# Optimization experiments

Hardware: AMD Instinct MI355X
Metric: run time of the kernel (lower is better)

Reference implementation:

```python
import jax, jax.numpy as jnp
import numpy as np

NUM_CLASSES = 81
TOP_K = 200
CONF_THRESH = 0.01
NMS_THRESH = 0.45
VAR0, VAR1 = 0.1, 0.2  # SSD Config['variance']


def decode(loc, priors):
    # loc: [..., P, 4], priors: [P, 4] (cx, cy, w, h)
    cxcy = priors[:, :2] + loc[..., :2] * VAR0 * priors[:, 2:]
    wh = priors[:, 2:] * jnp.exp(loc[..., 2:] * VAR1)
    x1y1 = cxcy - wh * 0.5
    x2y2 = x1y1 + wh
    return jnp.concatenate([x1y1, x2y2], axis=-1)  # [..., P, 4] xyxy


def nms_class(boxes, scores):
    # boxes: [P, 4], scores: [P] -> [TOP_K, 5] rows of (score, x1, y1, x2, y2)
    K = TOP_K
    masked = jnp.where(scores > CONF_THRESH, scores, -jnp.inf)
    top_scores, idx = jax.lax.top_k(masked, K)          # descending
    cand = boxes[idx]                                   # [K, 4]
    valid = jnp.isfinite(top_scores)
    x1, y1, x2, y2 = cand[:, 0], cand[:, 1], cand[:, 2], cand[:, 3]
    area = (x2 - x1) * (y2 - y1)
    iw = jnp.maximum(jnp.minimum(x2[:, None], x2[None, :]) - jnp.maximum(x1[:, None], x1[None, :]), 0.0)
    ih = jnp.maximum(jnp.minimum(y2[:, None], y2[None, :]) - jnp.maximum(y1[:, None], y1[None, :]), 0.0)
    inter = iw * ih
    union = area[:, None] + area[None, :] - inter
    iou = jnp.where(union > 0, inter / jnp.where(union > 0, union, 1.0), 0.0)  # [K, K]
    ar = jnp.arange(K)

    def step(suppressed, i):
        kept = valid[i] & ~suppressed[i]
        suppressed = suppressed | (kept & (iou[i] > NMS_THRESH) & (ar > i))
        return suppressed, kept

    _, keep = jax.lax.scan(step, jnp.zeros(K, dtype=bool), ar)  # [K] bool
    rows = jnp.concatenate([jnp.where(valid, top_scores, 0.0)[:, None], cand], axis=1)  # [K, 5]
    # compact kept rows to the front (score-descending order), zeros after
    tgt = jnp.where(keep, jnp.cumsum(keep) - 1, K)
    out = jnp.zeros((K + 1, 5), rows.dtype).at[tgt].set(rows)[:K]
    return out


def detect(loc_data, conf_data, prior_data):
    boxes = decode(loc_data, prior_data)                 # [B, P, 4]
    conf = jnp.transpose(conf_data, (0, 2, 1))           # [B, C, P]
    per_image = jax.vmap(nms_class, in_axes=(None, 0))   # over classes
    out = jax.vmap(per_image, in_axes=(0, 0))(boxes, conf)  # [B, C, K, 5]
    out = out.at[:, 0].set(0.0)  # background class skipped (cl starts at 1)
    return out


def setup_inputs() -> dict:
    key = jax.random.key(0)
    k1, k2, k3 = jax.random.split(key, 3)
    B, P, C = 32, 24564, NUM_CLASSES
    loc_data = jax.random.normal(k1, (B, P, 4), dtype=jnp.float32)
    conf_data = jax.random.uniform(k2, (B, P, C), dtype=jnp.float32)
    prior_data = jax.random.uniform(k3, (P, 4), dtype=jnp.float32)
    return {"loc_data": loc_data, "conf_data": conf_data, "prior_data": prior_data}


def reference(loc_data, conf_data, prior_data):
    return detect(loc_data, conf_data, prior_data)
```

## Files before the change

### kernel.cpp

```cpp
#include <hip/hip_runtime.h>
#include <hip/hip_bf16.h>
#include <math.h>

constexpr int B_ = 32;
constexpr int P_ = 24564;
constexpr int C_ = 81;
constexpr int K_ = 200;

constexpr int NCH = 64;
constexpr int CPR = 384;
constexpr int SCAP = 1024;
constexpr int CAP  = 512;
constexpr float T_SEL = 0.9869f;

__global__ __launch_bounds__(256) void k_filter(const float* __restrict__ conf,
                                                unsigned long long* __restrict__ cand,
                                                unsigned* __restrict__ cnt,
                                                unsigned* __restrict__ bflag) {
    __shared__ unsigned long long skey[SCAP];
    __shared__ unsigned short scls[SCAP];
    __shared__ unsigned scnt[C_], sbase[C_], scnt2[C_];
    __shared__ unsigned sn;
    const int bid = blockIdx.x;
    const int b = bid / NCH, ch = bid % NCH;
    const int tid = threadIdx.x;

    for (int i = tid; i < C_; i += 256) { scnt[i] = 0; scnt2[i] = 0; }
    if (tid == 0) sn = 0;
    __syncthreads();

    const int p0 = ch * CPR;
    const int rows = min(CPR, P_ - p0);
    const float* slab = conf + ((size_t)b * P_ + (size_t)p0) * C_;
    const int n4 = rows * C_ / 4;
    for (int g = tid; g < n4; g += 256) {
        float4 v = ((const float4*)slab)[g];
        int e = g * 4;
        int c = e % C_;
        int pl = e / C_;
        float s[4] = {v.x, v.y, v.z, v.w};
#pragma unroll
        for (int j = 0; j < 4; ++j) {
            int cj = c + j, pj = pl;
            if (cj >= C_) { cj -= C_; pj += 1; }
            float sv = s[j];
            if (sv > T_SEL && cj != 0) {
                unsigned pos = atomicAdd(&sn, 1u);
                if (pos < (unsigned)SCAP) {
                    unsigned pg = (unsigned)(p0 + pj);
                    skey[pos] = ((unsigned long long)__float_as_uint(sv) << 32) | (~pg);
                    scls[pos] = (unsigned short)cj;
                    atomicAdd(&scnt[cj], 1u);
                } else {
                    bflag[b] = 1u;
                }
            }
        }
    }
    __syncthreads();
    if (tid < C_) sbase[tid] = scnt[tid] ? atomicAdd(&cnt[b * C_ + tid], scnt[tid]) : 0u;
    __syncthreads();
    const int m = (int)min(sn, (unsigned)SCAP);
    for (int i = tid; i < m; i += 256) {
        int c = scls[i];
        unsigned pos = sbase[c] + atomicAdd(&scnt2[c], 1u);
        if (pos < (unsigned)CAP)
            cand[((size_t)(b * C_ + c)) * CAP + pos] = skey[i];
    }
}

__global__ __launch_bounds__(256) void k_nms(const unsigned long long* __restrict__ cand,
                                             const unsigned* __restrict__ cnt,
                                             const unsigned* __restrict__ bflag,
                                             const float* __restrict__ conf,
                                             const float* __restrict__ loc,
                                             const float* __restrict__ prior,
                                             float* __restrict__ out) {
#pragma clang fp contract(off)
    __shared__ __align__(16) unsigned long long masks[K_][4];
    __shared__ __align__(16) float outrow[1024];
    __shared__ __align__(16) unsigned long long top[256];
    __shared__ __align__(16) float4 bbox[K_];
    __shared__ float sc[K_], bar[K_];
    __shared__ unsigned char vflag[K_];
    __shared__ unsigned long long keepw[4];
    __shared__ unsigned kpre[4];
    __shared__ unsigned long long sh_prefix;
    __shared__ unsigned sh_rank, sh_cnt2, sh_cut, sh_fat;

    unsigned long long* buf = (unsigned long long*)outrow;
    unsigned* rs_hist = (unsigned*)&masks[0][0];
    unsigned* rs_sf   = (unsigned*)&masks[32][0];
    unsigned long long* srt = &masks[64][0];

    const int bid = blockIdx.x;
    const int b = bid / C_, c = bid % C_;
    const int tid = threadIdx.x;
    float* obase = out + ((size_t)(b * C_ + c)) * (K_ * 5);

    if (c == 0) {
        float4 z = make_float4(0.f, 0.f, 0.f, 0.f);
        for (int i = tid; i < K_ * 5 / 4; i += 256) ((float4*)obase)[i] = z;
        return;
    }

    const int task = b * C_ + c;
    const unsigned long long* crow = cand + (size_t)task * CAP;
    const unsigned cn = cnt[task];
    const bool fb = (bflag[b] != 0u) || (cn < (unsigned)K_) || (cn > (unsigned)CAP);

    int n;
    if (!fb) {
        n = (int)cn;
        for (int i = tid; i < CAP; i += 256)
            buf[i] = (i < n) ? crow[i] : 0ull;
        top[tid] = 0ull;
        rs_hist[tid] = 0u;
        __syncthreads();
    } else {
        for (int i = tid; i < CAP; i += 256) buf[i] = 0ull;
        top[tid] = 0ull;
        const float* col = conf + (size_t)b * P_ * C_ + c;
        unsigned lc = 0;
        for (int p = tid; p < P_; p += 256)
            if (col[(size_t)p * C_] > 0.01f) lc++;
        rs_sf[tid] = lc;
        __syncthreads();
        for (int off = 128; off > 0; off >>= 1) {
            if (tid < off) rs_sf[tid] += rs_sf[tid + off];
            __syncthreads();
        }
        const unsigned total = rs_sf[0];
        unsigned long long t200v = 1ull;
        if (total > (unsigned)K_) {
            if (tid == 0) { sh_prefix = 0ull; sh_rank = (unsigned)K_; }
            __syncthreads();
            for (int d = 7; d >= 0; --d) {
                rs_hist[tid] = 0;
                __syncthreads();
                const unsigned long long pref = sh_prefix;
                const unsigned rank = sh_rank;
                for (int p = tid; p < P_; p += 256) {
                    float sv = col[(size_t)p * C_];
                    if (sv > 0.01f) {
                        unsigned long long key =
                            ((unsigned long long)__float_as_uint(sv) << 32) | (~(unsigned)p);
                        bool match = (d == 7) || (((key ^ pref) >> ((d + 1) * 8)) == 0ull);
                        if (match) atomicAdd(&rs_hist[(unsigned)((key >> (d * 8)) & 255ull)], 1u);
                    }
                }
                __syncthreads();
                rs_sf[tid] = rs_hist[tid];
                __syncthreads();
                for (int off = 1; off < 256; off <<= 1) {
                    unsigned v2 = (tid + off < 256) ? rs_sf[tid + off] : 0u;
                    __syncthreads();
                    rs_sf[tid] += v2;
                    __syncthreads();
                }
                if (rs_sf[tid] >= rank && (tid == 255 || rs_sf[tid + 1] < rank)) {
                    sh_prefix = pref | ((unsigned long long)tid << (d * 8));
                    sh_rank = rank - ((tid == 255) ? 0u : rs_sf[tid + 1]);
                }
                __syncthreads();
            }
            t200v = sh_prefix;
        }
        if (tid == 0) sh_cnt2 = 0;
        __syncthreads();
        for (int p = tid; p < P_; p += 256) {
            float sv = col[(size_t)p * C_];
            if (sv > 0.01f) {
                unsigned long long key =
                    ((unsigned long long)__float_as_uint(sv) << 32) | (~(unsigned)p);
                if (key >= t200v) {
                    unsigned pos = atomicAdd(&sh_cnt2, 1u);
                    if (pos < (unsigned)CAP) buf[pos] = key;
                }
            }
        }
        __syncthreads();
        n = (int)min(sh_cnt2, (unsigned)CAP);
    }

    bool fat = false;
    if (n <= 256) {
        top[tid] = (tid < n) ? buf[tid] : 0ull;
        __syncthreads();
    } else {
        for (int i = tid; i < n; i += 256)
            atomicAdd(&rs_hist[(unsigned)((buf[i] >> 43) & 255ull)], 1u);
        __syncthreads();
        if (tid < 64) {
            const int l = tid;
            uint4 h = *(const uint4*)&rs_hist[l * 4];
            unsigned s3 = h.w;
            unsigned s2 = h.z + s3;
            unsigned s1 = h.y + s2;
            unsigned s0 = h.x + s1;
            unsigned acc = s0;
            for (int off = 1; off < 64; off <<= 1) {
                unsigned o = __shfl_down(acc, off, 64);
                if (l + off < 64) acc += o;
            }
            const unsigned suf_after = acc - s0;
            unsigned long long bal = __ballot(s0 + suf_after >= (unsigned)K_);
            int hl = 63 - __builtin_clzll(bal);
            if (l == hl) {
                int k; unsigned sufk;
                if      (s3 + suf_after >= (unsigned)K_) { k = 3; sufk = s3 + suf_after; }
                else if (s2 + suf_after >= (unsigned)K_) { k = 2; sufk = s2 + suf_after; }
                else if (s1 + suf_after >= (unsigned)K_) { k = 1; sufk = s1 + suf_after; }
                else                                     { k = 0; sufk = s0 + suf_after; }
                sh_cut = (unsigned)(l * 4 + k);
                sh_fat = (sufk > 256u) ? 1u : 0u;
                sh_cnt2 = 0u;
            }
        }
        __syncthreads();
        fat = (sh_fat != 0u);
        if (!fat) {
            const unsigned cut = sh_cut;
            for (int i = tid; i < n; i += 256) {
                unsigned long long key = buf[i];
                if ((unsigned)((key >> 43) & 255ull) >= cut)
                    top[atomicAdd(&sh_cnt2, 1u)] = key;
            }
            __syncthreads();
        }
    }

    if (!fat) {
        const unsigned long long k1 = top[tid];
        int r1 = 0;
        for (int i = 0; i < 256; i += 4) {
            ulonglong2 a  = *(const ulonglong2*)&top[i];
            ulonglong2 b2 = *(const ulonglong2*)&top[i + 2];
            r1 += (a.x > k1) + (a.y > k1) + (b2.x > k1) + (b2.y > k1);
        }
        if (k1 != 0ull) srt[r1] = k1;
    } else {
        const unsigned long long k1 = buf[tid];
        const unsigned long long k2 = buf[tid + 256];
        int r1 = 0, r2 = 0;
        for (int i = 0; i < 512; i += 4) {
            ulonglong2 a  = *(const ulonglong2*)&buf[i];
            ulonglong2 b2 = *(const ulonglong2*)&buf[i + 2];
            r1 += (a.x > k1) + (a.y > k1) + (b2.x > k1) + (b2.y > k1);
            r2 += (a.x > k2) + (a.y > k2) + (b2.x > k2) + (b2.y > k2);
        }
        if (k1 != 0ull && r1 < 256) srt[r1] = k1;
        if (k2 != 0ull && r2 < 256) srt[r2] = k2;
    }
    __syncthreads();

    const int nsel = min(n, K_);

    if (tid < K_) {
        const int r = tid;
        bool v = (r < nsel);
        float score = 0.f, x1 = 0.f, y1 = 0.f, x2 = 0.f, y2 = 0.f, ar = 0.f;
        if (v) {
            unsigned long long key = srt[r];
            unsigned ub = (unsigned)(key >> 32);
            unsigned p = ~((unsigned)key);
            score = __uint_as_float(ub);
            v = ((ub & 0x7F800000u) != 0x7F800000u);
            const float4 l4 = ((const float4*)loc)[(size_t)b * P_ + p];
            const float4 p4 = ((const float4*)prior)[p];
            float cx = p4.x + (l4.x * 0.1f) * p4.z;
            float cy = p4.y + (l4.y * 0.1f) * p4.w;
            float w  = p4.z * expf(l4.z * 0.2f);
            float h  = p4.w * expf(l4.w * 0.2f);
            x1 = cx - w * 0.5f;
            y1 = cy - h * 0.5f;
            x2 = x1 + w;
            y2 = y1 + h;
            ar = (x2 - x1) * (y2 - y1);
        }
        bbox[r] = make_float4(x1, y1, x2, y2);
        sc[r] = score; bar[r] = ar;
        vflag[r] = v ? (unsigned char)1 : (unsigned char)0;
    }
    __syncthreads();

    {
        float4 z = make_float4(0.f, 0.f, 0.f, 0.f);
        ((float4*)outrow)[tid] = z;
    }

    const int nv = nsel;
    const int wid = tid >> 6, lane = tid & 63;

    float4 jb[4]; float jar[4];
#pragma unroll
    for (int w = 0; w < 4; ++w) {
        int j = w * 64 + lane;
        bool in = (j < K_);
        jb[w]  = in ? bbox[j] : make_float4(0.f, 0.f, 0.f, 0.f);
        jar[w] = in ? bar[j] : 0.f;
    }

    for (int idx = tid; idx < K_ * 4; idx += 256) {
        int i = idx >> 2, w = idx & 3;
        if (w < (i >> 6)) masks[i][w] = 0ull;
    }
    for (int i = wid; i < nv; i += 4) {
        float4 rb = bbox[i];
        float r_ar = bar[i];
        const int w0 = i >> 6;
#pragma unroll
        for (int w = 0; w < 4; ++w) {
            if (w >= w0) {
                int j = w * 64 + lane;
                bool pred = false;
                if (j < nv && j > i) {
                    float xx1 = fmaxf(rb.x, jb[w].x);
                    float yy1 = fmaxf(rb.y, jb[w].y);
                    float xx2 = fminf(rb.z, jb[w].z);
                    float yy2 = fminf(rb.w, jb[w].w);
                    float iw = fmaxf(xx2 - xx1, 0.0f);
                    float ih = fmaxf(yy2 - yy1, 0.0f);
                    float inter = iw * ih;
                    float uni = (r_ar + jar[w]) - inter;
                    pred = (uni > 0.0f) && (inter / uni > 0.45f);
                }
                unsigned long long m = __ballot(pred);
                if (lane == 0) masks[i][w] = m;
            }
        }
    }
    __syncthreads();

    if (tid < 64) {
        const int l = tid;
        unsigned long long V0 = __ballot((l       < nv) && vflag[l]);
        unsigned long long V1 = __ballot((64 + l  < nv) && vflag[64 + l]);
        unsigned long long V2 = __ballot((128 + l < nv) && vflag[128 + l]);
        unsigned long long V3 = __ballot((192 + l < nv) && vflag[192 + l]);
        auto rownz = [&](int r) -> bool {
            if (r >= nv) return false;
            return (masks[r][0] | masks[r][1] | masks[r][2] | masks[r][3]) != 0ull;
        };
        unsigned long long R0 = __ballot(rownz(l))       & V0;
        unsigned long long R1 = __ballot(rownz(64 + l))  & V1;
        unsigned long long R2 = __ballot(rownz(128 + l)) & V2;
        unsigned long long R3 = __ballot(rownz(192 + l)) & V3;

        unsigned long long S0 = 0, S1 = 0, S2 = 0, S3 = 0;
        while (true) {
            unsigned long long t;
            int i = -1;
            if ((t = R0 & ~S0) != 0ull)      i = (int)__builtin_ctzll(t);
            else if ((t = R1 & ~S1) != 0ull) i = 64 + (int)__builtin_ctzll(t);
            else if ((t = R2 & ~S2) != 0ull) i = 128 + (int)__builtin_ctzll(t);
            else if ((t = R3 & ~S3) != 0ull) i = 192 + (int)__builtin_ctzll(t);
            if (i < 0) break;
            const unsigned long long bit = 1ull << (i & 63);
            const int slot = i >> 6;
            if (slot == 0) R0 ^= bit; else if (slot == 1) R1 ^= bit;
            else if (slot == 2) R2 ^= bit; else R3 ^= bit;
            ulonglong2 m01 = *(const ulonglong2*)&masks[i][0];
            ulonglong2 m23 = *(const ulonglong2*)&masks[i][2];
            S0 |= m01.x; S1 |= m01.y; S2 |= m23.x; S3 |= m23.y;
        }
        if (l == 0) {
            unsigned long long K0 = V0 & ~S0, K1 = V1 & ~S1, K2 = V2 & ~S2, K3 = V3 & ~S3;
            keepw[0] = K0; keepw[1] = K1; keepw[2] = K2; keepw[3] = K3;
            kpre[0] = 0;
            kpre[1] = (unsigned)__popcll(K0);
            kpre[2] = kpre[1] + (unsigned)__popcll(K1);
            kpre[3] = kpre[2] + (unsigned)__popcll(K2);
        }
    }
    __syncthreads();

    if (tid < nv) {
        int w = tid >> 6, bit = tid & 63;
        if ((keepw[w] >> bit) & 1ull) {
            unsigned slot = kpre[w] + (unsigned)__popcll(keepw[w] & ((1ull << bit) - 1ull));
            float4 bb = bbox[tid];
            outrow[slot * 5 + 0] = sc[tid];
            outrow[slot * 5 + 1] = bb.x;
            outrow[slot * 5 + 2] = bb.y;
            outrow[slot * 5 + 3] = bb.z;
            outrow[slot * 5 + 4] = bb.w;
        }
    }
    __syncthreads();

    for (int i = tid; i < K_ * 5 / 4; i += 256)
        ((float4*)obase)[i] = ((const float4*)outrow)[i];
}

extern "C" void kernel_launch(void* const* d_in, const int* in_sizes, int n_in,
                              void* d_out, int out_size, void* d_ws, size_t ws_size,
                              hipStream_t stream) {
    const float* loc   = (const float*)d_in[0];
    const float* conf  = (const float*)d_in[1];
    const float* prior = (const float*)d_in[2];
    float* out = (float*)d_out;

    char* ws = (char*)d_ws;
    const size_t candBytes = (size_t)B_ * C_ * CAP * sizeof(unsigned long long);
    unsigned long long* cand = (unsigned long long*)ws;
    unsigned* cnt   = (unsigned*)(ws + candBytes);
    unsigned* bflag = cnt + (size_t)B_ * C_;

    hipMemsetAsync(cnt, 0, (size_t)(B_ * C_ + B_) * sizeof(unsigned), stream);

    k_filter<<<B_ * NCH, 256, 0, stream>>>(conf, cand, cnt, bflag);
    k_nms   <<<B_ * C_,  256, 0, stream>>>(cand, cnt, bflag, conf, loc, prior, out);
}
```

Baseline: 156.7 us.

## Replace precomputed IoU mask matrix with on-the-fly greedy NMS in one wave

Drops the full K×K suppression-bitmask build and instead runs greedy NMS in a single wavefront, computing IoU only for rows that are actually kept and clearing suppressed bits via ballot. It also ranks candidates on the 32-bit score word with a tie-break pass, decodes boxes directly at their rank without an intermediate sorted array, compacts warp-wide with ballot instead of per-element atomics, and writes output straight to global memory while zero-filling only the tail. The cost removed is redundant IoU work and the extra shared-memory passes. In exchange the NMS loop becomes serial over kept boxes on just 64 threads, which could lengthen the critical path when many boxes are kept.

```diff
diff --git a/kernel.cpp b/kernel.cpp
--- a/kernel.cpp
+++ b/kernel.cpp
@@ -77,9 +77,9 @@
                                              const float* __restrict__ prior,
                                              float* __restrict__ out) {
 #pragma clang fp contract(off)
-    __shared__ __align__(16) unsigned long long masks[K_][4];
-    __shared__ __align__(16) float outrow[1024];
+    __shared__ __align__(16) unsigned long long buf[CAP];
     __shared__ __align__(16) unsigned long long top[256];
+    __shared__ __align__(16) unsigned shi[256];
     __shared__ __align__(16) float4 bbox[K_];
     __shared__ float sc[K_], bar[K_];
     __shared__ unsigned char vflag[K_];
@@ -88,14 +88,13 @@
     __shared__ unsigned long long sh_prefix;
     __shared__ unsigned sh_rank, sh_cnt2, sh_cut, sh_fat;
 
-    unsigned long long* buf = (unsigned long long*)outrow;
-    unsigned* rs_hist = (unsigned*)&masks[0][0];
-    unsigned* rs_sf   = (unsigned*)&masks[32][0];
-    unsigned long long* srt = &masks[64][0];
+    unsigned* rs_hist = (unsigned*)&bbox[0];
+    unsigned* rs_sf   = (unsigned*)&bbox[64];
 
     const int bid = blockIdx.x;
     const int b = bid / C_, c = bid % C_;
     const int tid = threadIdx.x;
+    const int lane = tid & 63;
     float* obase = out + ((size_t)(b * C_ + c)) * (K_ * 5);
 
     if (c == 0) {
@@ -110,16 +109,70 @@
     const bool fb = (bflag[b] != 0u) || (cn < (unsigned)K_) || (cn > (unsigned)CAP);
 
     int n;
+    bool fat = false;
     if (!fb) {
         n = (int)cn;
-        for (int i = tid; i < CAP; i += 256)
-            buf[i] = (i < n) ? crow[i] : 0ull;
-        top[tid] = 0ull;
-        rs_hist[tid] = 0u;
-        __syncthreads();
+        if (n <= 256) {
+            unsigned long long k = (tid < n) ? crow[tid] : 0ull;
+            top[tid] = k; shi[tid] = (unsigned)(k >> 32);
+            __syncthreads();
+        } else {
+            for (int i = tid; i < CAP; i += 256) buf[i] = (i < n) ? crow[i] : 0ull;
+            top[tid] = 0ull; shi[tid] = 0u; rs_hist[tid] = 0u;
+            __syncthreads();
+            for (int i = tid; i < n; i += 256)
+                atomicAdd(&rs_hist[(unsigned)((buf[i] >> 43) & 255ull)], 1u);
+            __syncthreads();
+            if (tid < 64) {
+                const int l = tid;
+                uint4 h = *(const uint4*)&rs_hist[l * 4];
+                unsigned s3 = h.w;
+                unsigned s2 = h.z + s3;
+                unsigned s1 = h.y + s2;
+                unsigned s0 = h.x + s1;
+                unsigned acc = s0;
+                for (int off = 1; off < 64; off <<= 1) {
+                    unsigned o = __shfl_down(acc, off, 64);
+                    if (l + off < 64) acc += o;
+                }
+                const unsigned suf_after = acc - s0;
+                unsigned long long bal = __ballot(s0 + suf_after >= (unsigned)K_);
+                int hl = 63 - __builtin_clzll(bal);
+                if (l == hl) {
+                    int k; unsigned sufk;
+                    if      (s3 + suf_after >= (unsigned)K_) { k = 3; sufk = s3 + suf_after; }
+                    else if (s2 + suf_after >= (unsigned)K_) { k = 2; sufk = s2 + suf_after; }
+                    else if (s1 + suf_after >= (unsigned)K_) { k = 1; sufk = s1 + suf_after; }
+                    else                                     { k = 0; sufk = s0 + suf_after; }
+                    sh_cut = (unsigned)(l * 4 + k);
+                    sh_fat = (sufk > 256u) ? 1u : 0u;
+                    sh_cnt2 = 0u;
+                }
+            }
+            __syncthreads();
+            fat = (sh_fat != 0u);
+            if (!fat) {
+                const unsigned cut = sh_cut;
+#pragma unroll
+                for (int base = 0; base < CAP; base += 256) {
+                    int i = base + tid;
+                    unsigned long long key = buf[i];
+                    bool q = (i < n) && ((unsigned)((key >> 43) & 255ull) >= cut);
+                    unsigned long long bal = __ballot(q);
+                    unsigned pre = (unsigned)__popcll(bal & ((1ull << lane) - 1ull));
+                    unsigned wb = 0;
+                    if (lane == 0) {
+                        unsigned cw = (unsigned)__popcll(bal);
+                        if (cw) wb = atomicAdd(&sh_cnt2, cw);
+                    }
+                    wb = (unsigned)__shfl((int)wb, 0, 64);
+                    if (q) { top[wb + pre] = key; shi[wb + pre] = (unsigned)(key >> 32); }
+                }
+                __syncthreads();
+            }
+        }
     } else {
         for (int i = tid; i < CAP; i += 256) buf[i] = 0ull;
-        top[tid] = 0ull;
         const float* col = conf + (size_t)b * P_ * C_ + c;
         unsigned lc = 0;
         for (int p = tid; p < P_; p += 256)
@@ -181,140 +234,113 @@
         }
         __syncthreads();
         n = (int)min(sh_cnt2, (unsigned)CAP);
-    }
-
-    bool fat = false;
-    if (n <= 256) {
-        top[tid] = (tid < n) ? buf[tid] : 0ull;
+        unsigned long long k = (tid < n) ? buf[tid] : 0ull;
+        top[tid] = k; shi[tid] = (unsigned)(k >> 32);
         __syncthreads();
-    } else {
-        for (int i = tid; i < n; i += 256)
-            atomicAdd(&rs_hist[(unsigned)((buf[i] >> 43) & 255ull)], 1u);
-        __syncthreads();
-        if (tid < 64) {
-            const int l = tid;
-            uint4 h = *(const uint4*)&rs_hist[l * 4];
-            unsigned s3 = h.w;
-            unsigned s2 = h.z + s3;
-            unsigned s1 = h.y + s2;
-            unsigned s0 = h.x + s1;
-            unsigned acc = s0;
-            for (int off = 1; off < 64; off <<= 1) {
-                unsigned o = __shfl_down(acc, off, 64);
-                if (l + off < 64) acc += o;
-            }
-            const unsigned suf_after = acc - s0;
-            unsigned long long bal = __ballot(s0 + suf_after >= (unsigned)K_);
-            int hl = 63 - __builtin_clzll(bal);
-            if (l == hl) {
-                int k; unsigned sufk;
-                if      (s3 + suf_after >= (unsigned)K_) { k = 3; sufk = s3 + suf_after; }
-                else if (s2 + suf_after >= (unsigned)K_) { k = 2; sufk = s2 + suf_after; }
-                else if (s1 + suf_after >= (unsigned)K_) { k = 1; sufk = s1 + suf_after; }
-                else                                     { k = 0; sufk = s0 + suf_after; }
-                sh_cut = (unsigned)(l * 4 + k);
-                sh_fat = (sufk > 256u) ? 1u : 0u;
-                sh_cnt2 = 0u;
-            }
-        }
-        __syncthreads();
-        fat = (sh_fat != 0u);
-        if (!fat) {
-            const unsigned cut = sh_cut;
-            for (int i = tid; i < n; i += 256) {
-                unsigned long long key = buf[i];
-                if ((unsigned)((key >> 43) & 255ull) >= cut)
-                    top[atomicAdd(&sh_cnt2, 1u)] = key;
-            }
-            __syncthreads();
-        }
-    }
+    }
+
+    const int nsel = min(n, K_);
+
+    auto decode_to = [&](unsigned long long key, int r) {
+        unsigned ub = (unsigned)(key >> 32);
+        unsigned p = ~((unsigned)key);
+        float score = __uint_as_float(ub);
+        bool v = ((ub & 0x7F800000u) != 0x7F800000u);
+        const float4 l4 = ((const float4*)loc)[(size_t)b * P_ + p];
+        const float4 p4 = ((const float4*)prior)[p];
+        float cx = p4.x + (l4.x * 0.1f) * p4.z;
+        float cy = p4.y + (l4.y * 0.1f) * p4.w;
+        float w  = p4.z * expf(l4.z * 0.2f);
+        float h  = p4.w * expf(l4.w * 0.2f);
+        float x1 = cx - w * 0.5f;
+        float y1 = cy - h * 0.5f;
+        float x2 = x1 + w;
+        float y2 = y1 + h;
+        bbox[r] = make_float4(x1, y1, x2, y2);
+        sc[r] = score;
+        bar[r] = (x2 - x1) * (y2 - y1);
+        vflag[r] = v ? (unsigned char)1 : (unsigned char)0;
+    };
 
     if (!fat) {
         const unsigned long long k1 = top[tid];
-        int r1 = 0;
-        for (int i = 0; i < 256; i += 4) {
-            ulonglong2 a  = *(const ulonglong2*)&top[i];
-            ulonglong2 b2 = *(const ulonglong2*)&top[i + 2];
-            r1 += (a.x > k1) + (a.y > k1) + (b2.x > k1) + (b2.y > k1);
-        }
-        if (k1 != 0ull) srt[r1] = k1;
+        const unsigned khi = (unsigned)(k1 >> 32);
+        int r1 = 0, eq = 0;
+        for (int i = 0; i < 256; i += 8) {
+            uint4 a = *(const uint4*)&shi[i];
+            uint4 d = *(const uint4*)&shi[i + 4];
+            r1 += (a.x > khi) + (a.y > khi) + (a.z > khi) + (a.w > khi)
+                + (d.x > khi) + (d.y > khi) + (d.z > khi) + (d.w > khi);
+            eq += (a.x == khi) + (a.y == khi) + (a.z == khi) + (a.w == khi)
+                + (d.x == khi) + (d.y == khi) + (d.z == khi) + (d.w == khi);
+        }
+        if (__any(k1 != 0ull && eq > 1)) {
+            const unsigned klo = (unsigned)k1;
+            for (int i = 0; i < 256; i += 4) {
+                ulonglong2 a = *(const ulonglong2*)&top[i];
+                ulonglong2 d = *(const ulonglong2*)&top[i + 2];
+                r1 += ((unsigned)(a.x >> 32) == khi) && ((unsigned)a.x > klo);
+                r1 += ((unsigned)(a.y >> 32) == khi) && ((unsigned)a.y > klo);
+                r1 += ((unsigned)(d.x >> 32) == khi) && ((unsigned)d.x > klo);
+                r1 += ((unsigned)(d.y >> 32) == khi) && ((unsigned)d.y > klo);
+            }
+        }
+        if (k1 != 0ull && r1 < K_) decode_to(k1, r1);
     } else {
         const unsigned long long k1 = buf[tid];
         const unsigned long long k2 = buf[tid + 256];
         int r1 = 0, r2 = 0;
-        for (int i = 0; i < 512; i += 4) {
-            ulonglong2 a  = *(const ulonglong2*)&buf[i];
-            ulonglong2 b2 = *(const ulonglong2*)&buf[i + 2];
-            r1 += (a.x > k1) + (a.y > k1) + (b2.x > k1) + (b2.y > k1);
-            r2 += (a.x > k2) + (a.y > k2) + (b2.x > k2) + (b2.y > k2);
-        }
-        if (k1 != 0ull && r1 < 256) srt[r1] = k1;
-        if (k2 != 0ull && r2 < 256) srt[r2] = k2;
+        for (int i = 0; i < CAP; i += 4) {
+            ulonglong2 a = *(const ulonglong2*)&buf[i];
+            ulonglong2 d = *(const ulonglong2*)&buf[i + 2];
+            r1 += (a.x > k1) + (a.y > k1) + (d.x > k1) + (d.y > k1);
+            r2 += (a.x > k2) + (a.y > k2) + (d.x > k2) + (d.y > k2);
+        }
+        if (k1 != 0ull && r1 < K_) decode_to(k1, r1);
+        if (k2 != 0ull && r2 < K_) decode_to(k2, r2);
+    }
+    if (tid >= nsel && tid < K_) {
+        bbox[tid] = make_float4(0.f, 0.f, 0.f, 0.f);
+        sc[tid] = 0.f; bar[tid] = 0.f; vflag[tid] = 0;
     }
     __syncthreads();
 
-    const int nsel = min(n, K_);
-
-    if (tid < K_) {
-        const int r = tid;
-        bool v = (r < nsel);
-        float score = 0.f, x1 = 0.f, y1 = 0.f, x2 = 0.f, y2 = 0.f, ar = 0.f;
-        if (v) {
-            unsigned long long key = srt[r];
-            unsigned ub = (unsigned)(key >> 32);
-            unsigned p = ~((unsigned)key);
-            score = __uint_as_float(ub);
-            v = ((ub & 0x7F800000u) != 0x7F800000u);
-            const float4 l4 = ((const float4*)loc)[(size_t)b * P_ + p];
-            const float4 p4 = ((const float4*)prior)[p];
-            float cx = p4.x + (l4.x * 0.1f) * p4.z;
-            float cy = p4.y + (l4.y * 0.1f) * p4.w;
-            float w  = p4.z * expf(l4.z * 0.2f);
-            float h  = p4.w * expf(l4.w * 0.2f);
-            x1 = cx - w * 0.5f;
-            y1 = cy - h * 0.5f;
-            x2 = x1 + w;
-            y2 = y1 + h;
-            ar = (x2 - x1) * (y2 - y1);
-        }
-        bbox[r] = make_float4(x1, y1, x2, y2);
-        sc[r] = score; bar[r] = ar;
-        vflag[r] = v ? (unsigned char)1 : (unsigned char)0;
-    }
-    __syncthreads();
-
-    {
-        float4 z = make_float4(0.f, 0.f, 0.f, 0.f);
-        ((float4*)outrow)[tid] = z;
-    }
-
-    const int nv = nsel;
-    const int wid = tid >> 6, lane = tid & 63;
-
-    float4 jb[4]; float jar[4];
-#pragma unroll
-    for (int w = 0; w < 4; ++w) {
-        int j = w * 64 + lane;
-        bool in = (j < K_);
-        jb[w]  = in ? bbox[j] : make_float4(0.f, 0.f, 0.f, 0.f);
-        jar[w] = in ? bar[j] : 0.f;
-    }
-
-    for (int idx = tid; idx < K_ * 4; idx += 256) {
-        int i = idx >> 2, w = idx & 3;
-        if (w < (i >> 6)) masks[i][w] = 0ull;
-    }
-    for (int i = wid; i < nv; i += 4) {
-        float4 rb = bbox[i];
-        float r_ar = bar[i];
-        const int w0 = i >> 6;
+    if (tid < 64) {
+        const int l = tid;
+        float4 jb[4]; float jar[4];
 #pragma unroll
         for (int w = 0; w < 4; ++w) {
-            if (w >= w0) {
-                int j = w * 64 + lane;
+            int j = w * 64 + l;
+            bool in = (j < K_);
+            jb[w]  = in ? bbox[j] : make_float4(0.f, 0.f, 0.f, 0.f);
+            jar[w] = in ? bar[j] : 0.f;
+        }
+        unsigned long long A0 = __ballot(vflag[l] != 0);
+        unsigned long long A1 = __ballot(vflag[64 + l] != 0);
+        unsigned long long A2 = __ballot(vflag[128 + l] != 0);
+        unsigned long long A3 = __ballot((192 + l < K_) && vflag[192 + l]);
+        unsigned long long K0 = 0, K1m = 0, K2m = 0, K3m = 0;
+
+        while (A0 | A1 | A2 | A3) {
+            int i;
+            if (A0)      i = (int)__builtin_ctzll(A0);
+            else if (A1) i = 64 + (int)__builtin_ctzll(A1);
+            else if (A2) i = 128 + (int)__builtin_ctzll(A2);
+            else         i = 192 + (int)__builtin_ctzll(A3);
+            const unsigned long long bit = 1ull << (i & 63);
+            const int slot = i >> 6;
+            if (slot == 0)      { A0 ^= bit; K0 |= bit; }
+            else if (slot == 1) { A1 ^= bit; K1m |= bit; }
+            else if (slot == 2) { A2 ^= bit; K2m |= bit; }
+            else                { A3 ^= bit; K3m |= bit; }
+
+            float4 rb = bbox[i];
+            float rar = bar[i];
+#pragma unroll
+            for (int w = 0; w < 4; ++w) {
+                int j = w * 64 + l;
                 bool pred = false;
-                if (j < nv && j > i) {
+                if (j > i) {
                     float xx1 = fmaxf(rb.x, jb[w].x);
                     float yy1 = fmaxf(rb.y, jb[w].y);
                     float xx2 = fminf(rb.z, jb[w].z);
@@ -322,75 +348,41 @@
                     float iw = fmaxf(xx2 - xx1, 0.0f);
                     float ih = fmaxf(yy2 - yy1, 0.0f);
                     float inter = iw * ih;
-                    float uni = (r_ar + jar[w]) - inter;
+                    float uni = (rar + jar[w]) - inter;
                     pred = (uni > 0.0f) && (inter / uni > 0.45f);
                 }
-                unsigned long long m = __ballot(pred);
-                if (lane == 0) masks[i][w] = m;
-            }
-        }
-    }
-    __syncthreads();
-
-    if (tid < 64) {
-        const int l = tid;
-        unsigned long long V0 = __ballot((l       < nv) && vflag[l]);
-        unsigned long long V1 = __ballot((64 + l  < nv) && vflag[64 + l]);
-        unsigned long long V2 = __ballot((128 + l < nv) && vflag[128 + l]);
-        unsigned long long V3 = __ballot((192 + l < nv) && vflag[192 + l]);
-        auto rownz = [&](int r) -> bool {
-            if (r >= nv) return false;
-            return (masks[r][0] | masks[r][1] | masks[r][2] | masks[r][3]) != 0ull;
-        };
-        unsigned long long R0 = __ballot(rownz(l))       & V0;
-        unsigned long long R1 = __ballot(rownz(64 + l))  & V1;
-        unsigned long long R2 = __ballot(rownz(128 + l)) & V2;
-        unsigned long long R3 = __ballot(rownz(192 + l)) & V3;
-
-        unsigned long long S0 = 0, S1 = 0, S2 = 0, S3 = 0;
-        while (true) {
-            unsigned long long t;
-            int i = -1;
-            if ((t = R0 & ~S0) != 0ull)      i = (int)__builtin_ctzll(t);
-            else if ((t = R1 & ~S1) != 0ull) i = 64 + (int)__builtin_ctzll(t);
-            else if ((t = R2 & ~S2) != 0ull) i = 128 + (int)__builtin_ctzll(t);
-            else if ((t = R3 & ~S3) != 0ull) i = 192 + (int)__builtin_ctzll(t);
-            if (i < 0) break;
-            const unsigned long long bit = 1ull << (i & 63);
-            const int slot = i >> 6;
-            if (slot == 0) R0 ^= bit; else if (slot == 1) R1 ^= bit;
-            else if (slot == 2) R2 ^= bit; else R3 ^= bit;
-            ulonglong2 m01 = *(const ulonglong2*)&masks[i][0];
-            ulonglong2 m23 = *(const ulonglong2*)&masks[i][2];
-            S0 |= m01.x; S1 |= m01.y; S2 |= m23.x; S3 |= m23.y;
+                unsigned long long bw = __ballot(pred);
+                if (w == 0) A0 &= ~bw;
+                else if (w == 1) A1 &= ~bw;
+                else if (w == 2) A2 &= ~bw;
+                else A3 &= ~bw;
+            }
         }
         if (l == 0) {
-            unsigned long long K0 = V0 & ~S0, K1 = V1 & ~S1, K2 = V2 & ~S2, K3 = V3 & ~S3;
-            keepw[0] = K0; keepw[1] = K1; keepw[2] = K2; keepw[3] = K3;
+            keepw[0] = K0; keepw[1] = K1m; keepw[2] = K2m; keepw[3] = K3m;
             kpre[0] = 0;
             kpre[1] = (unsigned)__popcll(K0);
-            kpre[2] = kpre[1] + (unsigned)__popcll(K1);
-            kpre[3] = kpre[2] + (unsigned)__popcll(K2);
+            kpre[2] = kpre[1] + (unsigned)__popcll(K1m);
+            kpre[3] = kpre[2] + (unsigned)__popcll(K2m);
         }
     }
     __syncthreads();
 
-    if (tid < nv) {
+    if (tid < K_) {
         int w = tid >> 6, bit = tid & 63;
         if ((keepw[w] >> bit) & 1ull) {
             unsigned slot = kpre[w] + (unsigned)__popcll(keepw[w] & ((1ull << bit) - 1ull));
             float4 bb = bbox[tid];
-            outrow[slot * 5 + 0] = sc[tid];
-            outrow[slot * 5 + 1] = bb.x;
-            outrow[slot * 5 + 2] = bb.y;
-            outrow[slot * 5 + 3] = bb.z;
-            outrow[slot * 5 + 4] = bb.w;
-        }
-    }
-    __syncthreads();
-
-    for (int i = tid; i < K_ * 5 / 4; i += 256)
-        ((float4*)obase)[i] = ((const float4*)outrow)[i];
+            float* o = obase + slot * 5;
+            o[0] = sc[tid]; o[1] = bb.x; o[2] = bb.y; o[3] = bb.z; o[4] = bb.w;
+        }
+    }
+    {
+        const unsigned keptTotal = kpre[3] + (unsigned)__popcll(keepw[3]);
+        const int zbase = (int)keptTotal * 5;
+        const int ztot = K_ * 5 - zbase;
+        for (int e = tid; e < ztot; e += 256) obase[zbase + e] = 0.0f;
+    }
 }
 
 extern "C" void kernel_launch(void* const* d_in, const int* in_sizes, int n_in,
```

Measured after the change: 212.5 us. 35.6% more time.

## Keep candidates in registers, fuse rank-sort with decode, write output directly

Applied to the files above, without the earlier changes.

In the fast path each thread now keeps its candidate keys in registers instead of staging them through shared memory. Compaction uses wave ballot plus one atomic per wave rather than per-element atomics. The rank computation writes decoded boxes straight into their sorted slot, which removes the separate srt array and one barrier. The shared outrow staging buffer is gone: kept rows go directly to global memory and only the tail is zero-filled. The IoU test switches from a float divide to a double-precision compare against a midpoint threshold, which trades the divide for double arithmetic while aiming to reproduce the float rounding.

```diff
diff --git a/kernel.cpp b/kernel.cpp
--- a/kernel.cpp
+++ b/kernel.cpp
@@ -78,7 +78,6 @@
                                              float* __restrict__ out) {
 #pragma clang fp contract(off)
     __shared__ __align__(16) unsigned long long masks[K_][4];
-    __shared__ __align__(16) float outrow[1024];
     __shared__ __align__(16) unsigned long long top[256];
     __shared__ __align__(16) float4 bbox[K_];
     __shared__ float sc[K_], bar[K_];
@@ -88,14 +87,14 @@
     __shared__ unsigned long long sh_prefix;
     __shared__ unsigned sh_rank, sh_cnt2, sh_cut, sh_fat;
 
-    unsigned long long* buf = (unsigned long long*)outrow;
-    unsigned* rs_hist = (unsigned*)&masks[0][0];
-    unsigned* rs_sf   = (unsigned*)&masks[32][0];
-    unsigned long long* srt = &masks[64][0];
+    unsigned long long* buf = &masks[0][0];
+    unsigned* rs_hist = (unsigned*)&masks[128][0];
+    unsigned* rs_sf   = (unsigned*)&masks[160][0];
 
     const int bid = blockIdx.x;
     const int b = bid / C_, c = bid % C_;
     const int tid = threadIdx.x;
+    const int lane = tid & 63;
     float* obase = out + ((size_t)(b * C_ + c)) * (K_ * 5);
 
     if (c == 0) {
@@ -110,16 +109,85 @@
     const bool fb = (bflag[b] != 0u) || (cn < (unsigned)K_) || (cn > (unsigned)CAP);
 
     int n;
+    bool fat = false;
     if (!fb) {
         n = (int)cn;
-        for (int i = tid; i < CAP; i += 256)
-            buf[i] = (i < n) ? crow[i] : 0ull;
-        top[tid] = 0ull;
-        rs_hist[tid] = 0u;
-        __syncthreads();
+        const unsigned long long k1 = (tid < n)       ? crow[tid]       : 0ull;
+        const unsigned long long k2 = (tid + 256 < n) ? crow[tid + 256] : 0ull;
+        if (n <= 256) {
+            top[tid] = k1;
+            __syncthreads();
+        } else {
+            rs_hist[tid] = 0u;
+            top[tid] = 0ull;
+            __syncthreads();
+            atomicAdd(&rs_hist[(unsigned)((k1 >> 43) & 255ull)], 1u);
+            if (tid + 256 < n)
+                atomicAdd(&rs_hist[(unsigned)((k2 >> 43) & 255ull)], 1u);
+            __syncthreads();
+            if (tid < 64) {
+                const int l = tid;
+                uint4 h = *(const uint4*)&rs_hist[l * 4];
+                unsigned s3 = h.w;
+                unsigned s2 = h.z + s3;
+                unsigned s1 = h.y + s2;
+                unsigned s0 = h.x + s1;
+                unsigned acc = s0;
+                for (int off = 1; off < 64; off <<= 1) {
+                    unsigned o = __shfl_down(acc, off, 64);
+                    if (l + off < 64) acc += o;
+                }
+                const unsigned suf_after = acc - s0;
+                unsigned long long bal = __ballot(s0 + suf_after >= (unsigned)K_);
+                int hl = 63 - __builtin_clzll(bal);
+                if (l == hl) {
+                    int k; unsigned sufk;
+                    if      (s3 + suf_after >= (unsigned)K_) { k = 3; sufk = s3 + suf_after; }
+                    else if (s2 + suf_after >= (unsigned)K_) { k = 2; sufk = s2 + suf_after; }
+                    else if (s1 + suf_after >= (unsigned)K_) { k = 1; sufk = s1 + suf_after; }
+                    else                                     { k = 0; sufk = s0 + suf_after; }
+                    sh_cut = (unsigned)(l * 4 + k);
+                    sh_fat = (sufk > 256u) ? 1u : 0u;
+                    sh_cnt2 = 0u;
+                }
+            }
+            __syncthreads();
+            fat = (sh_fat != 0u);
+            if (!fat) {
+                const unsigned cut = sh_cut;
+                {
+                    bool q = ((unsigned)((k1 >> 43) & 255ull) >= cut);
+                    unsigned long long bal = __ballot(q);
+                    unsigned pre = (unsigned)__popcll(bal & ((1ull << lane) - 1ull));
+                    unsigned wb = 0;
+                    if (lane == 0) {
+                        unsigned cw = (unsigned)__popcll(bal);
+                        if (cw) wb = atomicAdd(&sh_cnt2, cw);
+                    }
+                    wb = (unsigned)__shfl((int)wb, 0, 64);
+                    if (q) top[wb + pre] = k1;
+                }
+                {
+                    bool q = (tid + 256 < n) && ((unsigned)((k2 >> 43) & 255ull) >= cut);
+                    unsigned long long bal = __ballot(q);
+                    unsigned pre = (unsigned)__popcll(bal & ((1ull << lane) - 1ull));
+                    unsigned wb = 0;
+                    if (lane == 0) {
+                        unsigned cw = (unsigned)__popcll(bal);
+                        if (cw) wb = atomicAdd(&sh_cnt2, cw);
+                    }
+                    wb = (unsigned)__shfl((int)wb, 0, 64);
+                    if (q) top[wb + pre] = k2;
+                }
+                __syncthreads();
+            } else {
+                buf[tid] = k1;
+                buf[tid + 256] = k2;
+                __syncthreads();
+            }
+        }
     } else {
         for (int i = tid; i < CAP; i += 256) buf[i] = 0ull;
-        top[tid] = 0ull;
         const float* col = conf + (size_t)b * P_ * C_ + c;
         unsigned lc = 0;
         for (int p = tid; p < P_; p += 256)
@@ -181,116 +249,66 @@
         }
         __syncthreads();
         n = (int)min(sh_cnt2, (unsigned)CAP);
-    }
-
-    bool fat = false;
-    if (n <= 256) {
         top[tid] = (tid < n) ? buf[tid] : 0ull;
         __syncthreads();
-    } else {
-        for (int i = tid; i < n; i += 256)
-            atomicAdd(&rs_hist[(unsigned)((buf[i] >> 43) & 255ull)], 1u);
-        __syncthreads();
-        if (tid < 64) {
-            const int l = tid;
-            uint4 h = *(const uint4*)&rs_hist[l * 4];
-            unsigned s3 = h.w;
-            unsigned s2 = h.z + s3;
-            unsigned s1 = h.y + s2;
-            unsigned s0 = h.x + s1;
-            unsigned acc = s0;
-            for (int off = 1; off < 64; off <<= 1) {
-                unsigned o = __shfl_down(acc, off, 64);
-                if (l + off < 64) acc += o;
-            }
-            const unsigned suf_after = acc - s0;
-            unsigned long long bal = __ballot(s0 + suf_after >= (unsigned)K_);
-            int hl = 63 - __builtin_clzll(bal);
-            if (l == hl) {
-                int k; unsigned sufk;
-                if      (s3 + suf_after >= (unsigned)K_) { k = 3; sufk = s3 + suf_after; }
-                else if (s2 + suf_after >= (unsigned)K_) { k = 2; sufk = s2 + suf_after; }
-                else if (s1 + suf_after >= (unsigned)K_) { k = 1; sufk = s1 + suf_after; }
-                else                                     { k = 0; sufk = s0 + suf_after; }
-                sh_cut = (unsigned)(l * 4 + k);
-                sh_fat = (sufk > 256u) ? 1u : 0u;
-                sh_cnt2 = 0u;
-            }
-        }
-        __syncthreads();
-        fat = (sh_fat != 0u);
-        if (!fat) {
-            const unsigned cut = sh_cut;
-            for (int i = tid; i < n; i += 256) {
-                unsigned long long key = buf[i];
-                if ((unsigned)((key >> 43) & 255ull) >= cut)
-                    top[atomicAdd(&sh_cnt2, 1u)] = key;
-            }
-            __syncthreads();
-        }
-    }
+    }
+
+    const int nsel = min(n, K_);
+
+    auto decode_to = [&](unsigned long long key, int r) {
+        unsigned ub = (unsigned)(key >> 32);
+        unsigned p = ~((unsigned)key);
+        float score = __uint_as_float(ub);
+        bool v = ((ub & 0x7F800000u) != 0x7F800000u);
+        const float4 l4 = ((const float4*)loc)[(size_t)b * P_ + p];
+        const float4 p4 = ((const float4*)prior)[p];
+        float cx = p4.x + (l4.x * 0.1f) * p4.z;
+        float cy = p4.y + (l4.y * 0.1f) * p4.w;
+        float w  = p4.z * expf(l4.z * 0.2f);
+        float h  = p4.w * expf(l4.w * 0.2f);
+        float x1 = cx - w * 0.5f;
+        float y1 = cy - h * 0.5f;
+        float x2 = x1 + w;
+        float y2 = y1 + h;
+        bbox[r] = make_float4(x1, y1, x2, y2);
+        sc[r] = score;
+        bar[r] = (x2 - x1) * (y2 - y1);
+        vflag[r] = v ? (unsigned char)1 : (unsigned char)0;
+    };
 
     if (!fat) {
-        const unsigned long long k1 = top[tid];
-        int r1 = 0;
+        const unsigned long long k = top[tid];
+        int r = 0;
+#pragma unroll 4
         for (int i = 0; i < 256; i += 4) {
-            ulonglong2 a  = *(const ulonglong2*)&top[i];
-            ulonglong2 b2 = *(const ulonglong2*)&top[i + 2];
-            r1 += (a.x > k1) + (a.y > k1) + (b2.x > k1) + (b2.y > k1);
-        }
-        if (k1 != 0ull) srt[r1] = k1;
+            ulonglong2 a = *(const ulonglong2*)&top[i];
+            ulonglong2 d = *(const ulonglong2*)&top[i + 2];
+            r += (a.x > k) + (a.y > k) + (d.x > k) + (d.y > k);
+        }
+        if (k != 0ull && r < K_) decode_to(k, r);
     } else {
         const unsigned long long k1 = buf[tid];
         const unsigned long long k2 = buf[tid + 256];
         int r1 = 0, r2 = 0;
-        for (int i = 0; i < 512; i += 4) {
-            ulonglong2 a  = *(const ulonglong2*)&buf[i];
-            ulonglong2 b2 = *(const ulonglong2*)&buf[i + 2];
-            r1 += (a.x > k1) + (a.y > k1) + (b2.x > k1) + (b2.y > k1);
-            r2 += (a.x > k2) + (a.y > k2) + (b2.x > k2) + (b2.y > k2);
-        }
-        if (k1 != 0ull && r1 < 256) srt[r1] = k1;
-        if (k2 != 0ull && r2 < 256) srt[r2] = k2;
-    }
-    __syncthreads();
-
-    const int nsel = min(n, K_);
-
-    if (tid < K_) {
-        const int r = tid;
-        bool v = (r < nsel);
-        float score = 0.f, x1 = 0.f, y1 = 0.f, x2 = 0.f, y2 = 0.f, ar = 0.f;
-        if (v) {
-            unsigned long long key = srt[r];
-            unsigned ub = (unsigned)(key >> 32);
-            unsigned p = ~((unsigned)key);
-            score = __uint_as_float(ub);
-            v = ((ub & 0x7F800000u) != 0x7F800000u);
-            const float4 l4 = ((const float4*)loc)[(size_t)b * P_ + p];
-            const float4 p4 = ((const float4*)prior)[p];
-            float cx = p4.x + (l4.x * 0.1f) * p4.z;
-            float cy = p4.y + (l4.y * 0.1f) * p4.w;
-            float w  = p4.z * expf(l4.z * 0.2f);
-            float h  = p4.w * expf(l4.w * 0.2f);
-            x1 = cx - w * 0.5f;
-            y1 = cy - h * 0.5f;
-            x2 = x1 + w;
-            y2 = y1 + h;
-            ar = (x2 - x1) * (y2 - y1);
-        }
-        bbox[r] = make_float4(x1, y1, x2, y2);
-        sc[r] = score; bar[r] = ar;
-        vflag[r] = v ? (unsigned char)1 : (unsigned char)0;
-    }
-    __syncthreads();
-
-    {
-        float4 z = make_float4(0.f, 0.f, 0.f, 0.f);
-        ((float4*)outrow)[tid] = z;
-    }
-
+        for (int i = 0; i < CAP; i += 4) {
+            ulonglong2 a = *(const ulonglong2*)&buf[i];
+            ulonglong2 d = *(const ulonglong2*)&buf[i + 2];
+            r1 += (a.x > k1) + (a.y > k1) + (d.x > k1) + (d.y > k1);
+            r2 += (a.x > k2) + (a.y > k2) + (d.x > k2) + (d.y > k2);
+        }
+        if (k1 != 0ull && r1 < K_) decode_to(k1, r1);
+        if (k2 != 0ull && r2 < K_) decode_to(k2, r2);
+    }
+    if (tid >= nsel && tid < K_) {
+        bbox[tid] = make_float4(0.f, 0.f, 0.f, 0.f);
+        sc[tid] = 0.f; bar[tid] = 0.f; vflag[tid] = 0;
+    }
+    __syncthreads();
+
+    const double M_IOU = 0.5 * ((double)__uint_as_float(0x3EE66666u) +
+                                (double)__uint_as_float(0x3EE66667u));
     const int nv = nsel;
-    const int wid = tid >> 6, lane = tid & 63;
+    const int wid = tid >> 6;
 
     float4 jb[4]; float jar[4];
 #pragma unroll
@@ -323,7 +341,7 @@
                     float ih = fmaxf(yy2 - yy1, 0.0f);
                     float inter = iw * ih;
                     float uni = (r_ar + jar[w]) - inter;
-                    pred = (uni > 0.0f) && (inter / uni > 0.45f);
+                    pred = (uni > 0.0f) && ((double)inter > M_IOU * (double)uni);
                 }
                 unsigned long long m = __ballot(pred);
                 if (lane == 0) masks[i][w] = m;
@@ -375,22 +393,21 @@
     }
     __syncthreads();
 
-    if (tid < nv) {
+    if (tid < K_) {
         int w = tid >> 6, bit = tid & 63;
         if ((keepw[w] >> bit) & 1ull) {
             unsigned slot = kpre[w] + (unsigned)__popcll(keepw[w] & ((1ull << bit) - 1ull));
             float4 bb = bbox[tid];
-            outrow[slot * 5 + 0] = sc[tid];
-            outrow[slot * 5 + 1] = bb.x;
-            outrow[slot * 5 + 2] = bb.y;
-            outrow[slot * 5 + 3] = bb.z;
-            outrow[slot * 5 + 4] = bb.w;
-        }
-    }
-    __syncthreads();
-
-    for (int i = tid; i < K_ * 5 / 4; i += 256)
-        ((float4*)obase)[i] = ((const float4*)outrow)[i];
+            float* o = obase + slot * 5;
+            o[0] = sc[tid]; o[1] = bb.x; o[2] = bb.y; o[3] = bb.z; o[4] = bb.w;
+        }
+    }
+    {
+        const unsigned keptTotal = kpre[3] + (unsigned)__popcll(keepw[3]);
+        const int zbase = (int)keptTotal * 5;
+        const int ztot = K_ * 5 - zbase;
+        for (int e = tid; e < ztot; e += 256) obase[zbase + e] = 0.0f;
+    }
 }
 
 extern "C" void kernel_launch(void* const* d_in, const int* in_sizes, int n_in,
```

Result: faster. 147.9 us (-5.6%).
